# Kernel optimization log

Measured on AMD Instinct MI355X. Metric: run time of the kernel, lower is better.

The kernel has to match this reference:

```python
import jax, jax.numpy as jnp
import numpy as np

N_NODES = 50000
N_EDGES = 800000
D_IN = 512
D_OUT = 512


def setup_inputs() -> dict:
    key = jax.random.key(0)
    k1, k2, k3, k4, k5 = jax.random.split(key, 5)
    adj_rows = jnp.sort(jax.random.randint(k1, (N_EDGES,), 0, N_NODES, dtype=jnp.int32))
    adj_cols = jax.random.randint(k2, (N_EDGES,), 0, N_NODES, dtype=jnp.int32)
    adj_vals = jax.random.uniform(k3, (N_EDGES,), dtype=jnp.float32)
    u_f = jax.random.normal(k4, (N_NODES, D_IN), dtype=jnp.float32)
    # xavier_uniform init for weight [in_feats, out_feats]
    limit = float(np.sqrt(6.0 / (D_IN + D_OUT)))
    weight = jax.random.uniform(k5, (D_IN, D_OUT), dtype=jnp.float32, minval=-limit, maxval=limit)
    return {"adj_rows": adj_rows, "adj_cols": adj_cols, "adj_vals": adj_vals,
            "u_f": u_f, "weight": weight}


def reference(adj_rows, adj_cols, adj_vals, u_f, weight):
    # dense projection: [N, d_in] @ [d_in, d_out] -> [N, d_out]
    h = u_f @ weight
    # sparse adj (COO) @ h: gather source rows, scale by edge vals, scatter-add to dest rows
    msgs = adj_vals[:, None] * h[adj_cols]              # [E, d_out]
    out = jax.ops.segment_sum(msgs, adj_rows, num_segments=N_NODES)  # [N, d_out]
    return jax.nn.relu(out)
```

## Files before the change

### kernel.cpp

```cpp
#include <hip/hip_runtime.h>
#include <cstdint>
#include <cstddef>

#define N_NODES 50000
#define N_EDGES 800000
#define D 512
#define M_PAD 50048

typedef __bf16 bf16x8 __attribute__((ext_vector_type(8)));
typedef float floatx4 __attribute__((ext_vector_type(4)));

typedef const __attribute__((address_space(1))) unsigned int* gas_u32p;
typedef __attribute__((address_space(3))) unsigned int* las_u32p;

__device__ __forceinline__ unsigned short f2bf(float f) {
    unsigned int u = __builtin_bit_cast(unsigned int, f);
    u += 0x7FFFu + ((u >> 16) & 1u);
    return (unsigned short)(u >> 16);
}
__device__ __forceinline__ float bflo(unsigned int u) {
    return __builtin_bit_cast(float, u << 16);
}
__device__ __forceinline__ float bfhi(unsigned int u) {
    return __builtin_bit_cast(float, u & 0xFFFF0000u);
}

__global__ __launch_bounds__(256) void k_convert_u(const float* __restrict__ u,
                                                   unsigned short* __restrict__ ub) {
    size_t i = (size_t)blockIdx.x * 256 + threadIdx.x;
    size_t base = i * 8;
    if (base >= (size_t)M_PAD * D) return;
    uint4 o;
    if (base < (size_t)N_NODES * D) {
        const float4* s = (const float4*)(u + base);
        float4 a = s[0], b = s[1];
        o.x = (unsigned)f2bf(a.x) | ((unsigned)f2bf(a.y) << 16);
        o.y = (unsigned)f2bf(a.z) | ((unsigned)f2bf(a.w) << 16);
        o.z = (unsigned)f2bf(b.x) | ((unsigned)f2bf(b.y) << 16);
        o.w = (unsigned)f2bf(b.z) | ((unsigned)f2bf(b.w) << 16);
    } else {
        o = make_uint4(0u, 0u, 0u, 0u);
    }
    *(uint4*)(ub + base) = o;
}

__global__ __launch_bounds__(256) void k_convert_wt(const float* __restrict__ w,
                                                    unsigned short* __restrict__ wt) {
    int id = blockIdx.x * 256 + threadIdx.x;
    int n = id >> 9, k = id & 511;
    wt[id] = f2bf(w[k * D + n]);
}

__global__ __launch_bounds__(256) void k_rowptr(const int* __restrict__ rows,
                                                int* __restrict__ rp) {
    int i = blockIdx.x * 256 + threadIdx.x;
    if (i > N_NODES) return;
    int lo = 0, hi = N_EDGES;
    while (lo < hi) {
        int mid = (lo + hi) >> 1;
        if (rows[mid] < i) lo = mid + 1; else hi = mid;
    }
    rp[i] = lo;
}

__global__ __launch_bounds__(256) void k_gemm(const unsigned short* __restrict__ A,
                                              const unsigned short* __restrict__ WT,
                                              unsigned short* __restrict__ H) {
    __shared__ unsigned short lA[128 * 32];
    __shared__ unsigned short lB[128 * 32];
    int b = blockIdx.x;
    int mt, nt;
    if (b < 1536) {
        mt = (b >> 5) * 8 + (b & 7);
        nt = (b >> 3) & 3;
    } else {
        int r = b - 1536;
        mt = 384 + (r % 7);
        nt = r / 7;
    }
    const int tid  = threadIdx.x;
    const int wave = tid >> 6, lane = tid & 63;
    const int tileM0 = mt * 128;
    const int tileN0 = nt * 128;
    const int wr = wave >> 1, wc = wave & 1;

    const int lrow = lane >> 2, lslot = lane & 3;
    const int r0 = wave * 32;
    const int m0 = r0 + lrow,      m1 = r0 + 16 + lrow;
    const int q0 = (lslot - (m0 >> 1)) & 3;
    const int q1 = (lslot - (m1 >> 1)) & 3;
    const unsigned short* gA0 = A  + (size_t)(tileM0 + m0) * D + q0 * 8;
    const unsigned short* gA1 = A  + (size_t)(tileM0 + m1) * D + q1 * 8;
    const unsigned short* gB0 = WT + (size_t)(tileN0 + m0) * D + q0 * 8;
    const unsigned short* gB1 = WT + (size_t)(tileN0 + m1) * D + q1 * 8;
    unsigned short* lA0 = lA + r0 * 32;
    unsigned short* lA1 = lA + (r0 + 16) * 32;
    unsigned short* lB0 = lB + r0 * 32;
    unsigned short* lB1 = lB + (r0 + 16) * 32;

    floatx4 acc[4][4] = {};

    const int quad = lane >> 4, half = lane & 15;
    int offA[4], offB[4];
#pragma unroll
    for (int i = 0; i < 4; i++) {
        int m = wr * 64 + i * 16 + half;
        offA[i] = m * 32 + ((quad + (m >> 1)) & 3) * 8;
        int n = wc * 64 + i * 16 + half;
        offB[i] = n * 32 + ((quad + (n >> 1)) & 3) * 8;
    }

    for (int k0 = 0; k0 < D; k0 += 32) {
        __syncthreads();
        __builtin_amdgcn_global_load_lds((gas_u32p)(gA0 + k0), (las_u32p)lA0, 16, 0, 0);
        __builtin_amdgcn_global_load_lds((gas_u32p)(gA1 + k0), (las_u32p)lA1, 16, 0, 0);
        __builtin_amdgcn_global_load_lds((gas_u32p)(gB0 + k0), (las_u32p)lB0, 16, 0, 0);
        __builtin_amdgcn_global_load_lds((gas_u32p)(gB1 + k0), (las_u32p)lB1, 16, 0, 0);
        __syncthreads();

        bf16x8 af[4], bfr[4];
#pragma unroll
        for (int i = 0; i < 4; i++) {
            af[i]  = *(const bf16x8*)(lA + offA[i]);
            bfr[i] = *(const bf16x8*)(lB + offB[i]);
        }
#pragma unroll
        for (int i = 0; i < 4; i++)
#pragma unroll
            for (int j = 0; j < 4; j++)
                acc[i][j] = __builtin_amdgcn_mfma_f32_16x16x32_bf16(af[i], bfr[j], acc[i][j], 0, 0, 0);
    }

#pragma unroll
    for (int i = 0; i < 4; i++) {
        int gm0 = tileM0 + wr * 64 + i * 16 + quad * 4;
#pragma unroll
        for (int j = 0; j < 4; j++) {
            int gn = tileN0 + wc * 64 + j * 16 + half;
#pragma unroll
            for (int r = 0; r < 4; r++) {
                H[(size_t)(gm0 + r) * D + gn] = f2bf(acc[i][j][r]);
            }
        }
    }
}

__global__ __launch_bounds__(256) void k_scatter_half(const int* __restrict__ rp,
                                                      const int* __restrict__ cols,
                                                      const float* __restrict__ vals,
                                                      const unsigned short* __restrict__ H,
                                                      float* __restrict__ out,
                                                      int node_base) {
    int node = node_base + (int)((blockIdx.x * 256 + threadIdx.x) >> 6);
    int lane = threadIdx.x & 63;
    if (node >= N_NODES) return;
    int s = rp[node], e = rp[node + 1];
    float a0 = 0.f, a1 = 0.f, a2 = 0.f, a3 = 0.f;
    float a4 = 0.f, a5 = 0.f, a6 = 0.f, a7 = 0.f;
    const uint4* H4 = (const uint4*)H;
    const int lq = lane;
    for (int t = s; t < e; t += 4) {
        int last = e - 1;
        int t1 = t + 1 < e ? t + 1 : last;
        int t2 = t + 2 < e ? t + 2 : last;
        int t3 = t + 3 < e ? t + 3 : last;
        int c0 = cols[t],  c1 = cols[t1], c2 = cols[t2], c3 = cols[t3];
        float v0 = vals[t];
        float v1 = t + 1 < e ? vals[t1] : 0.f;
        float v2 = t + 2 < e ? vals[t2] : 0.f;
        float v3 = t + 3 < e ? vals[t3] : 0.f;
        uint4 d0 = H4[(size_t)c0 * 64 + lq];
        uint4 d1 = H4[(size_t)c1 * 64 + lq];
        uint4 d2 = H4[(size_t)c2 * 64 + lq];
        uint4 d3 = H4[(size_t)c3 * 64 + lq];
        a0 = fmaf(v0, bflo(d0.x), a0); a1 = fmaf(v0, bfhi(d0.x), a1);
        a2 = fmaf(v0, bflo(d0.y), a2); a3 = fmaf(v0, bfhi(d0.y), a3);
        a4 = fmaf(v0, bflo(d0.z), a4); a5 = fmaf(v0, bfhi(d0.z), a5);
        a6 = fmaf(v0, bflo(d0.w), a6); a7 = fmaf(v0, bfhi(d0.w), a7);
        a0 = fmaf(v1, bflo(d1.x), a0); a1 = fmaf(v1, bfhi(d1.x), a1);
        a2 = fmaf(v1, bflo(d1.y), a2); a3 = fmaf(v1, bfhi(d1.y), a3);
        a4 = fmaf(v1, bflo(d1.z), a4); a5 = fmaf(v1, bfhi(d1.z), a5);
        a6 = fmaf(v1, bflo(d1.w), a6); a7 = fmaf(v1, bfhi(d1.w), a7);
        a0 = fmaf(v2, bflo(d2.x), a0); a1 = fmaf(v2, bfhi(d2.x), a1);
        a2 = fmaf(v2, bflo(d2.y), a2); a3 = fmaf(v2, bfhi(d2.y), a3);
        a4 = fmaf(v2, bflo(d2.z), a4); a5 = fmaf(v2, bfhi(d2.z), a5);
        a6 = fmaf(v2, bflo(d2.w), a6); a7 = fmaf(v2, bfhi(d2.w), a7);
        a0 = fmaf(v3, bflo(d3.x), a0); a1 = fmaf(v3, bfhi(d3.x), a1);
        a2 = fmaf(v3, bflo(d3.y), a2); a3 = fmaf(v3, bfhi(d3.y), a3);
        a4 = fmaf(v3, bflo(d3.z), a4); a5 = fmaf(v3, bfhi(d3.z), a5);
        a6 = fmaf(v3, bflo(d3.w), a6); a7 = fmaf(v3, bfhi(d3.w), a7);
    }
    float* o = out + (size_t)node * D + (size_t)lane * 8;
    *(float4*)o       = make_float4(fmaxf(a0, 0.f), fmaxf(a1, 0.f), fmaxf(a2, 0.f), fmaxf(a3, 0.f));
    *(float4*)(o + 4) = make_float4(fmaxf(a4, 0.f), fmaxf(a5, 0.f), fmaxf(a6, 0.f), fmaxf(a7, 0.f));
}

extern "C" void kernel_launch(void* const* d_in, const int* in_sizes, int n_in,
                              void* d_out, int out_size, void* d_ws, size_t ws_size,
                              hipStream_t stream) {
    const int*   adj_rows = (const int*)d_in[0];
    const int*   adj_cols = (const int*)d_in[1];
    const float* adj_vals = (const float*)d_in[2];
    const float* u_f      = (const float*)d_in[3];
    const float* weight   = (const float*)d_in[4];
    float* out = (float*)d_out;

    char* ws = (char*)d_ws;
    unsigned short* wt_bf = (unsigned short*)ws;
    unsigned short* h_bf  = (unsigned short*)(ws + 524288);
    int* rowptr           = (int*)(ws + 524288 + 51249152);

    unsigned short* u_bf = (unsigned short*)d_out;

    hipLaunchKernelGGL(k_convert_u,  dim3(12512), dim3(256), 0, stream, u_f, u_bf);
    hipLaunchKernelGGL(k_convert_wt, dim3(1024),  dim3(256), 0, stream, weight, wt_bf);
    hipLaunchKernelGGL(k_rowptr,     dim3(196),   dim3(256), 0, stream, adj_rows, rowptr);
    hipLaunchKernelGGL(k_gemm,       dim3(1564),  dim3(256), 0, stream, u_bf, wt_bf, h_bf);
    hipLaunchKernelGGL(k_scatter_half, dim3(6250), dim3(256), 0, stream, rowptr, adj_cols, adj_vals, h_bf, out, 0);
    hipLaunchKernelGGL(k_scatter_half, dim3(6250), dim3(256), 0, stream, rowptr, adj_cols, adj_vals, h_bf, out, 25000);
}
```

Measured before the change: 204.5 us.

## Fuse fp32-to-bf16 conversion of u_f into GEMM A-tile loads

Removes the separate k_convert_u pass that wrote a bf16 copy of u_f into the output buffer. The GEMM now loads fp32 A rows directly with float4 reads, converts them to bf16 in registers and stores them into LDS, with bounds masking replacing the zero padding. This saves a full read and write of the activation matrix, but the GEMM now reads twice as many A bytes and loses the async global_load_lds path for A. It also merges the two half scatter launches into one.

```diff
diff --git a/kernel.cpp b/kernel.cpp
--- a/kernel.cpp
+++ b/kernel.cpp
@@ -24,24 +24,11 @@
 __device__ __forceinline__ float bfhi(unsigned int u) {
     return __builtin_bit_cast(float, u & 0xFFFF0000u);
 }
-
-__global__ __launch_bounds__(256) void k_convert_u(const float* __restrict__ u,
-                                                   unsigned short* __restrict__ ub) {
-    size_t i = (size_t)blockIdx.x * 256 + threadIdx.x;
-    size_t base = i * 8;
-    if (base >= (size_t)M_PAD * D) return;
-    uint4 o;
-    if (base < (size_t)N_NODES * D) {
-        const float4* s = (const float4*)(u + base);
-        float4 a = s[0], b = s[1];
-        o.x = (unsigned)f2bf(a.x) | ((unsigned)f2bf(a.y) << 16);
-        o.y = (unsigned)f2bf(a.z) | ((unsigned)f2bf(a.w) << 16);
-        o.z = (unsigned)f2bf(b.x) | ((unsigned)f2bf(b.y) << 16);
-        o.w = (unsigned)f2bf(b.z) | ((unsigned)f2bf(b.w) << 16);
-    } else {
-        o = make_uint4(0u, 0u, 0u, 0u);
-    }
-    *(uint4*)(ub + base) = o;
+__device__ __forceinline__ bf16x8 cvt8(float4 lo, float4 hi) {
+    bf16x8 r;
+    r[0] = (__bf16)lo.x; r[1] = (__bf16)lo.y; r[2] = (__bf16)lo.z; r[3] = (__bf16)lo.w;
+    r[4] = (__bf16)hi.x; r[5] = (__bf16)hi.y; r[6] = (__bf16)hi.z; r[7] = (__bf16)hi.w;
+    return r;
 }
 
 __global__ __launch_bounds__(256) void k_convert_wt(const float* __restrict__ w,
@@ -63,7 +50,7 @@
     rp[i] = lo;
 }
 
-__global__ __launch_bounds__(256) void k_gemm(const unsigned short* __restrict__ A,
+__global__ __launch_bounds__(256) void k_gemm(const float* __restrict__ Af,
                                               const unsigned short* __restrict__ WT,
                                               unsigned short* __restrict__ H) {
     __shared__ unsigned short lA[128 * 32];
@@ -89,12 +76,14 @@
     const int m0 = r0 + lrow,      m1 = r0 + 16 + lrow;
     const int q0 = (lslot - (m0 >> 1)) & 3;
     const int q1 = (lslot - (m1 >> 1)) & 3;
-    const unsigned short* gA0 = A  + (size_t)(tileM0 + m0) * D + q0 * 8;
-    const unsigned short* gA1 = A  + (size_t)(tileM0 + m1) * D + q1 * 8;
+    const bool ok0 = (tileM0 + m0) < N_NODES;
+    const bool ok1 = (tileM0 + m1) < N_NODES;
+    const float* gAf0 = Af + (size_t)(tileM0 + m0) * D + q0 * 8;
+    const float* gAf1 = Af + (size_t)(tileM0 + m1) * D + q1 * 8;
     const unsigned short* gB0 = WT + (size_t)(tileN0 + m0) * D + q0 * 8;
     const unsigned short* gB1 = WT + (size_t)(tileN0 + m1) * D + q1 * 8;
-    unsigned short* lA0 = lA + r0 * 32;
-    unsigned short* lA1 = lA + (r0 + 16) * 32;
+    unsigned short* wA0 = lA + m0 * 32 + lslot * 8;
+    unsigned short* wA1 = lA + m1 * 32 + lslot * 8;
     unsigned short* lB0 = lB + r0 * 32;
     unsigned short* lB1 = lB + (r0 + 16) * 32;
 
@@ -111,11 +100,15 @@
     }
 
     for (int k0 = 0; k0 < D; k0 += 32) {
+        float4 z = make_float4(0.f, 0.f, 0.f, 0.f);
+        float4 a0lo = z, a0hi = z, a1lo = z, a1hi = z;
+        if (ok0) { a0lo = *(const float4*)(gAf0 + k0); a0hi = *(const float4*)(gAf0 + k0 + 4); }
+        if (ok1) { a1lo = *(const float4*)(gAf1 + k0); a1hi = *(const float4*)(gAf1 + k0 + 4); }
         __syncthreads();
-        __builtin_amdgcn_global_load_lds((gas_u32p)(gA0 + k0), (las_u32p)lA0, 16, 0, 0);
-        __builtin_amdgcn_global_load_lds((gas_u32p)(gA1 + k0), (las_u32p)lA1, 16, 0, 0);
         __builtin_amdgcn_global_load_lds((gas_u32p)(gB0 + k0), (las_u32p)lB0, 16, 0, 0);
         __builtin_amdgcn_global_load_lds((gas_u32p)(gB1 + k0), (las_u32p)lB1, 16, 0, 0);
+        *(bf16x8*)wA0 = cvt8(a0lo, a0hi);
+        *(bf16x8*)wA1 = cvt8(a1lo, a1hi);
         __syncthreads();
 
         bf16x8 af[4], bfr[4];
@@ -145,13 +138,12 @@
     }
 }
 
-__global__ __launch_bounds__(256) void k_scatter_half(const int* __restrict__ rp,
-                                                      const int* __restrict__ cols,
-                                                      const float* __restrict__ vals,
-                                                      const unsigned short* __restrict__ H,
-                                                      float* __restrict__ out,
-                                                      int node_base) {
-    int node = node_base + (int)((blockIdx.x * 256 + threadIdx.x) >> 6);
+__global__ __launch_bounds__(256) void k_scatter(const int* __restrict__ rp,
+                                                 const int* __restrict__ cols,
+                                                 const float* __restrict__ vals,
+                                                 const unsigned short* __restrict__ H,
+                                                 float* __restrict__ out) {
+    int node = (int)((blockIdx.x * 256 + threadIdx.x) >> 6);
     int lane = threadIdx.x & 63;
     if (node >= N_NODES) return;
     int s = rp[node], e = rp[node + 1];
@@ -210,12 +202,8 @@
     unsigned short* h_bf  = (unsigned short*)(ws + 524288);
     int* rowptr           = (int*)(ws + 524288 + 51249152);
 
-    unsigned short* u_bf = (unsigned short*)d_out;
-
-    hipLaunchKernelGGL(k_convert_u,  dim3(12512), dim3(256), 0, stream, u_f, u_bf);
     hipLaunchKernelGGL(k_convert_wt, dim3(1024),  dim3(256), 0, stream, weight, wt_bf);
     hipLaunchKernelGGL(k_rowptr,     dim3(196),   dim3(256), 0, stream, adj_rows, rowptr);
-    hipLaunchKernelGGL(k_gemm,       dim3(1564),  dim3(256), 0, stream, u_bf, wt_bf, h_bf);
-    hipLaunchKernelGGL(k_scatter_half, dim3(6250), dim3(256), 0, stream, rowptr, adj_cols, adj_vals, h_bf, out, 0);
-    hipLaunchKernelGGL(k_scatter_half, dim3(6250), dim3(256), 0, stream, rowptr, adj_cols, adj_vals, h_bf, out, 25000);
-}
+    hipLaunchKernelGGL(k_gemm,       dim3(1564),  dim3(256), 0, stream, u_f, wt_bf, h_bf);
+    hipLaunchKernelGGL(k_scatter,    dim3(12500), dim3(256), 0, stream, rowptr, adj_cols, adj_vals, h_bf, out);
+}
```

Measured after the change: 207.4 us. No clear change (+1.4%).
